# Kernel optimization log

Measured on AMD Instinct MI355X. Metric: run time of the kernel, lower is better.

## Reference

```python
import jax, jax.numpy as jnp
import numpy as np

B, T, ZS, ZT, H = 256, 256, 128, 64, 512
TAU = 1.0  # gumbel temperature


def setup_inputs() -> dict:
    key = jax.random.key(0)
    ks = iter(jax.random.split(key, 40))
    s = 0.05
    p = lambda shape: s * jax.random.normal(next(ks), shape, jnp.float32)
    return {
        'z_static': jax.random.normal(next(ks), (B, ZS), jnp.float32),
        'z_temporal': jax.random.normal(next(ks), (B, T, ZT), jnp.float32),
        'fc1_w': p((H, ZS)), 'fc1_b': p((H,)),
        'fc2_w': p((H, H)), 'fc2_b': p((H,)),
        'w_ih0': p((3 * H, ZT + H)), 'w_hh0': p((3 * H, H)), 'b_ih0': p((3 * H,)), 'b_hh0': p((3 * H,)),
        'w_ih1': p((3 * H, H)), 'w_hh1': p((3 * H, H)), 'b_ih1': p((3 * H,)), 'b_hh1': p((3 * H,)),
        'time_w': p((1, H)), 'time_b': p((1,)),
        'visit_w': p((1, H)), 'visit_b': p((1,)),
        'tcont_w': p((32, H)), 'tcont_b': p((32,)),
        'irr0_w': p((1, H)), 'irr0_b': p((1,)),
        'irr1_w': p((1, H)), 'irr1_b': p((1,)),
        'cat0_w': p((8, H)), 'cat0_b': p((8,)),
        'cat1_w': p((16, H)), 'cat1_b': p((16,)),
        'scont_w': p((16, H)), 'scont_b': p((16,)),
        'scat_w': p((10, H)), 'scat_b': p((10,)),
    }


def _gru_layer(x, w_ih, w_hh, b_ih, b_hh):
    # x: [B, T, in] -> [B, T, H]. PyTorch GRU gate order: r, z, n.
    xp = jnp.einsum('bti,gi->btg', x, w_ih) + b_ih  # [B,T,3H]
    h0 = jnp.zeros((x.shape[0], w_hh.shape[1]), x.dtype)

    def step(h, xpt):
        gh = h @ w_hh.T + b_hh
        ir, iz, inn = jnp.split(xpt, 3, axis=-1)
        hr, hz, hn = jnp.split(gh, 3, axis=-1)
        r = jax.nn.sigmoid(ir + hr)
        z = jax.nn.sigmoid(iz + hz)
        n = jnp.tanh(inn + r * hn)
        h = (1.0 - z) * n + z * h
        return h, h

    _, hs = jax.lax.scan(step, h0, xp.transpose(1, 0, 2))
    return hs.transpose(1, 0, 2)


def _gumbel_hard(k, logits, tau):
    u = jax.random.uniform(k, logits.shape, jnp.float32, 1e-9, 1.0)
    g = -jnp.log(-jnp.log(u))
    y = jax.nn.softmax((logits + g) / tau, axis=-1)
    hard = jax.nn.one_hot(jnp.argmax(y, axis=-1), logits.shape[-1], dtype=y.dtype)
    return hard + y - jax.lax.stop_gradient(y)  # straight-through


def _irr_scan(hazard, u):
    # hazard, u: [B, T] -> irreversible 0->1 states [B, T]
    def step(prev, hu):
        h, uu = hu
        flip = (uu < h * (1.0 - prev)).astype(h.dtype)
        prev = prev + flip
        return prev, prev

    _, st = jax.lax.scan(step, jnp.zeros(hazard.shape[0], hazard.dtype),
                         (hazard.T, u.T))
    return st.T


def reference(z_static, z_temporal, fc1_w, fc1_b, fc2_w, fc2_b,
              w_ih0, w_hh0, b_ih0, b_hh0, w_ih1, w_hh1, b_ih1, b_hh1,
              time_w, time_b, visit_w, visit_b, tcont_w, tcont_b,
              irr0_w, irr0_b, irr1_w, irr1_b, cat0_w, cat0_b, cat1_w, cat1_b,
              scont_w, scont_b, scat_w, scat_b):
    rk = jax.random.key(42)
    k_visit, k_i0, k_i1, k_c0, k_c1, k_sc = jax.random.split(rk, 6)

    static_h = jax.nn.relu(z_static @ fc1_w.T + fc1_b) @ fc2_w.T + fc2_b  # [B,H]
    gru_in = jnp.concatenate(
        [z_temporal, jnp.broadcast_to(static_h[:, None, :], (B, T, H))], axis=-1)
    h1 = _gru_layer(gru_in, w_ih0, w_hh0, b_ih0, b_hh0)
    h_seq = _gru_layer(h1, w_ih1, w_hh1, b_ih1, b_hh1)  # [B,T,H]

    static_cont = static_h @ scont_w.T + scont_b
    static_cat = _gumbel_hard(k_sc, static_h @ scat_w.T + scat_b, TAU)

    delta_t = jax.nn.softplus(jnp.squeeze(h_seq @ time_w.T + time_b, -1))  # [B,T]
    visit_times = jnp.cumsum(delta_t, axis=1)
    visit_times = visit_times / (jnp.max(visit_times, axis=1, keepdims=True) + 1e-8)

    visit_prob = jax.nn.sigmoid(jnp.squeeze(h_seq @ visit_w.T + visit_b, -1))
    u_visit = jax.random.uniform(k_visit, (B, T), jnp.float32)
    vm = (u_visit < visit_prob).astype(jnp.float32)
    vm = vm.at[:, 0].set(1.0)
    visit_mask = jnp.cumprod(vm, axis=1)[..., None]  # [B,T,1] monotone mask

    temporal_cont = (h_seq @ tcont_w.T + tcont_b) * visit_mask

    # irreversible categoricals via hazard recurrence
    def irr_out(w, b, k):
        hz = jax.nn.sigmoid(jnp.squeeze(h_seq @ w.T + b, -1))  # [B,T]
        st = _irr_scan(hz, jax.random.uniform(k, (B, T), jnp.float32))
        return jnp.stack([1.0 - st, st], axis=-1) * visit_mask  # [B,T,2]

    irr0 = irr_out(irr0_w, irr0_b, k_i0)
    irr1 = irr_out(irr1_w, irr1_b, k_i1)

    cat0 = _gumbel_hard(k_c0, h_seq @ cat0_w.T + cat0_b, TAU) * visit_mask
    cat1 = _gumbel_hard(k_c1, h_seq @ cat1_w.T + cat1_b, TAU) * visit_mask

    return (static_cont, static_cat, temporal_cont, irr0, irr1, cat0, cat1,
            visit_mask, visit_times)
```

## Files before the change

kernel.cpp:

```cpp
#include <hip/hip_runtime.h>
#include <hip/hip_bf16.h>
#include <cstdint>
#include <cstddef>

#define RNG_PART 1

typedef __bf16 bf16x8 __attribute__((ext_vector_type(8)));
typedef float f32x4 __attribute__((ext_vector_type(4)));
typedef unsigned short ushort_t;


static constexpr size_t ACC0 = 0;
static constexpr size_t SHH  = 393216;
static constexpr size_t HID  = 524288;
static constexpr size_t H0F  = 655360;
static constexpr size_t H1F  = 917504;
static constexpr size_t LOGB = 1179648;
static constexpr size_t WTH  = 5373952;
static constexpr size_t H0S  = 5406720;
static constexpr size_t H1S  = 5799936;
static constexpr size_t WB1  = 6193152;
static constexpr size_t WA0  = 8552448;
static constexpr size_t WH   = 9879552;
static constexpr size_t FC1T = LOGB;
static constexpr size_t FC2T = LOGB + 65536;
static constexpr size_t WIS  = FC2T + 262144;

static constexpr size_t O_SCONT = 0;
static constexpr size_t O_SCAT  = 4096;
static constexpr size_t O_TCONT = 6656;
static constexpr size_t O_IRR0  = 2103808;
static constexpr size_t O_IRR1  = 2234880;
static constexpr size_t O_CAT0  = 2365952;
static constexpr size_t O_CAT1  = 2890240;
static constexpr size_t O_VMASK = 3938816;
static constexpr size_t O_VTIME = 4004352;

__host__ __device__ inline void tf2x32(unsigned k0, unsigned k1, unsigned x0, unsigned x1,
                                       unsigned* o0, unsigned* o1) {
  unsigned ks2 = k0 ^ k1 ^ 0x1BD11BDAu;
#define TFR(r) { x0 += x1; x1 = (x1 << (r)) | (x1 >> (32 - (r))); x1 ^= x0; }
  x0 += k0; x1 += k1;
  TFR(13) TFR(15) TFR(26) TFR(6)
  x0 += k1; x1 += ks2 + 1u;
  TFR(17) TFR(29) TFR(16) TFR(24)
  x0 += ks2; x1 += k0 + 2u;
  TFR(13) TFR(15) TFR(26) TFR(6)
  x0 += k0; x1 += k1 + 3u;
  TFR(17) TFR(29) TFR(16) TFR(24)
  x0 += k1; x1 += ks2 + 4u;
  TFR(13) TFR(15) TFR(26) TFR(6)
  x0 += ks2; x1 += k0 + 5u;
#undef TFR
  *o0 = x0; *o1 = x1;
}

__device__ inline float rng_u01(unsigned k0, unsigned k1, unsigned idx) {
  unsigned o0, o1;
  tf2x32(k0, k1, 0u, idx, &o0, &o1);
  unsigned bits = o0 ^ o1;
  return __uint_as_float((bits >> 9) | 0x3f800000u) - 1.0f;
}

__device__ inline float sigmoidf_(float x) { return 1.0f / (1.0f + expf(-x)); }

__global__ __launch_bounds__(256) void transpose_k(const float* __restrict__ src, float* __restrict__ dst,
                                                   int J, int K, int srcStride, int dstStride) {
  __shared__ float tile[32][33];
  int kb = blockIdx.x * 32, jb = blockIdx.y * 32;
  int tx = threadIdx.x & 31, ty = threadIdx.x >> 5;
  #pragma unroll
  for (int r = 0; r < 4; ++r) {
    int j = jb + ty + r * 8, k = kb + tx;
    if (j < J && k < K) tile[ty + r * 8][tx] = src[(size_t)j * srcStride + k];
  }
  __syncthreads();
  #pragma unroll
  for (int r = 0; r < 4; ++r) {
    int k = kb + ty + r * 8, j = jb + tx;
    if (k < K && j < J) dst[(size_t)k * dstStride + j] = tile[tx][ty + r * 8];
  }
}

__global__ void hgather_k(const float* __restrict__ time_w, const float* __restrict__ visit_w,
                          const float* __restrict__ tcont_w, const float* __restrict__ irr0_w,
                          const float* __restrict__ irr1_w, const float* __restrict__ cat0_w,
                          const float* __restrict__ cat1_w, float* __restrict__ wtH) {
  int c = blockIdx.x;
  if (c >= 60) {
    for (int k = threadIdx.x; k < 512; k += blockDim.x) wtH[(size_t)k * 64 + c] = 0.0f;
    return;
  }
  const float* src;
  if (c == 0) src = time_w;
  else if (c == 1) src = visit_w;
  else if (c < 34) src = tcont_w + (size_t)(c - 2) * 512;
  else if (c == 34) src = irr0_w;
  else if (c == 35) src = irr1_w;
  else if (c < 44) src = cat0_w + (size_t)(c - 36) * 512;
  else src = cat1_w + (size_t)(c - 44) * 512;
  for (int k = threadIdx.x; k < 512; k += blockDim.x) wtH[(size_t)k * 64 + c] = src[k];
}

__global__ __launch_bounds__(128) void gemm_k(const float* __restrict__ in, const float* __restrict__ wT,
                                              const float* __restrict__ bias, float* __restrict__ out,
                                              int M, int K, int J, int relu) {
  __shared__ float ibuf[64][34];
  __shared__ float wbuf[64][36];
  int jt = blockIdx.x % (J >> 5), mt = blockIdx.x / (J >> 5);
  int m0 = mt * 32, j0 = jt * 32;
  int tid = threadIdx.x;
  int mq = tid & 15, jq = tid >> 4;
  float acc[2][4] = {{0.f, 0.f, 0.f, 0.f}, {0.f, 0.f, 0.f, 0.f}};
  for (int kc = 0; kc < K; kc += 64) {
    __syncthreads();
    #pragma unroll
    for (int i = 0; i < 16; ++i) {
      int lin = i * 128 + tid;
// ... 40 lines not shown
                                                   ushort_t* __restrict__ dst) {
  int id = blockIdx.x * 256 + threadIdx.x;
  if (id >= 32 * 32 * 3 * 64) return;
  int l = id & 63; int rest = id >> 6;
  int g = rest % 3; rest /= 3;
  int ht = rest & 31; int kc = rest >> 5;
  int n = g * 512 + ht * 16 + (l & 15);
  int kbase = kc * 32 + (l >> 4) * 8;
  size_t ob = (size_t)((kc * 32 + ht) * 3 + g) * 1536 + (size_t)l * 8;
  #pragma unroll
  for (int j = 0; j < 8; ++j) {
    int k = kbase + j;
    float v = (k < 512) ? w_ih1[(size_t)n * 512 + k] : w_hh1[(size_t)n * 512 + (k - 512)];
    split3_store(v, dst + ob + j, dst + ob + 512 + j, dst + ob + 1024 + j);
  }
}

__global__ __launch_bounds__(256) void arrangeA0_k(const float* __restrict__ w_hh0,
                                                   const float* __restrict__ w_ih0,
                                                   ushort_t* __restrict__ dst) {
  int id = blockIdx.x * 256 + threadIdx.x;
  if (id >= 18 * 32 * 3 * 64) return;
  int l = id & 63; int rest = id >> 6;
  int g = rest % 3; rest /= 3;
  int ht = rest & 31; int kc = rest >> 5;
  int n = g * 512 + ht * 16 + (l & 15);
  int kbase = kc * 32 + (l >> 4) * 8;
  size_t ob = (size_t)((kc * 32 + ht) * 3 + g) * 1536 + (size_t)l * 8;
  #pragma unroll
  for (int j = 0; j < 8; ++j) {
    int k = kbase + j;
    float v = (k < 512) ? w_hh0[(size_t)n * 512 + k] : w_ih0[(size_t)n * 576 + (k - 512)];
    split3_store(v, dst + ob + j, dst + ob + 512 + j, dst + ob + 1024 + j);
  }
}

__global__ __launch_bounds__(256) void arrangeH_k(const float* __restrict__ wtH,
                                                  ushort_t* __restrict__ dst) {
  int id = blockIdx.x * 256 + threadIdx.x;
  if (id >= 16 * 4 * 64) return;
  int l = id & 63; int rest = id >> 6;
  int ct = rest & 3; int kc = rest >> 2;
  int c = ct * 16 + (l & 15);
  int kbase = kc * 32 + (l >> 4) * 8;
  size_t ob = (size_t)(kc * 4 + ct) * 1536 + (size_t)l * 8;
  #pragma unroll
  for (int j = 0; j < 8; ++j) {
    float v = wtH[(size_t)(kbase + j) * 64 + c];
    split3_store(v, dst + ob + j, dst + ob + 512 + j, dst + ob + 1024 + j);
  }
}

__device__ inline bf16x8 ldb8(const ushort_t* p) { return *reinterpret_cast<const bf16x8*>(p); }

#define MFMA_(A, W, C) __builtin_amdgcn_mfma_f32_16x16x32_bf16((A), (W), (C), 0, 0, 0)

__device__ inline f32x4 mm6(f32x4 acc, bf16x8 a0, bf16x8 a1, bf16x8 a2, const ushort_t* wb) {
  bf16x8 w0 = ldb8(wb), w1 = ldb8(wb + 512), w2 = ldb8(wb + 1024);
  acc = MFMA_(a0, w0, acc); acc = MFMA_(a0, w1, acc); acc = MFMA_(a1, w0, acc);
  acc = MFMA_(a1, w1, acc); acc = MFMA_(a0, w2, acc); acc = MFMA_(a2, w0, acc);
  return acc;
}

struct HeadPtrs {
  const float *time_b, *visit_b, *tcont_b, *irr0_b, *irr1_b, *cat0_b, *cat1_b;
};

__device__ inline float head_bias(const HeadPtrs& hp, int c) {
  if (c == 0) return hp.time_b[0];
  if (c == 1) return hp.visit_b[0];
  if (c < 34) return hp.tcont_b[c - 2];
  if (c == 34) return hp.irr0_b[0];
  if (c == 35) return hp.irr1_b[0];
  if (c < 44) return hp.cat0_b[c - 36];
  return hp.cat1_b[c - 44];
}

__global__ __launch_bounds__(256, 2) void step_k(int s,
    const float* __restrict__ z_temporal,
    const float* __restrict__ b_hh0,
    const float* __restrict__ b_ih1, const float* __restrict__ b_hh1,
    float* __restrict__ ws, HeadPtrs hp)
{
  __shared__ f32x4 red[2][4][64];
  const int blk = blockIdx.x, tid = threadIdx.x;
  const int wv = tid >> 6, l = tid & 63, lm = l & 15, lq = l >> 4;
  const int mt = wv & 1, kh = wv >> 1;
  const ushort_t* h0sAll = (const ushort_t*)(ws + H0S);
  const ushort_t* h1sAll = (const ushort_t*)(ws + H1S);

  if (blk < 512) {
    const int job = blk & 1;
    const int idx = blk >> 1;
    const int ht = idx & 31, bt = idx >> 5;
    const int b0 = bt * 32 + mt * 16;
    const int hc = ht * 16;
    const size_t arow = (size_t)(b0 + lm) * 512 + (size_t)lq * 8;

    if (job == 0) {
      if (s < 1 || s > 256) return;
      const ushort_t* act = (kh == 0) ? (h0sAll + (size_t)((s - 1) & 1) * 393216)
                                      : (h1sAll + (size_t)(s & 1) * 393216);
      const ushort_t* wbB = (const ushort_t*)(ws + WB1) + (size_t)ht * 4608 + (size_t)l * 8
                            + (size_t)(kh * 16) * 147456;
      f32x4 vr = {}, vz = {}, vn = {};
      #pragma unroll 2
      for (int kcl = 0; kcl < 16; ++kcl) {
        const size_t ao = arow + (size_t)kcl * 32;
        bf16x8 a0 = ldb8(act + ao);
        bf16x8 a1 = ldb8(act + 131072 + ao);
        bf16x8 a2 = ldb8(act + 262144 + ao);
        const ushort_t* wb = wbB + (size_t)kcl * 147456;
        vr = mm6(vr, a0, a1, a2, wb);
        vz = mm6(vz, a0, a1, a2, wb + 1536);
        vn = mm6(vn, a0, a1, a2, wb + 3072);
      }
      if (kh == 1) { red[mt][0][l] = vr; red[mt][1][l] = vz; red[mt][2][l] = vn; }
      __syncthreads();
      if (kh == 0) {
        const f32x4 r4 = vr + red[mt][0][l];
        const f32x4 z4 = vz + red[mt][1][l];
        const f32x4 nh4 = red[mt][2][l];
        const float* h1f_old = ws + H1F + (size_t)(s & 1) * 131072;
        float* h1f_cur = ws + H1F + (size_t)((s - 1) & 1) * 131072;
        ushort_t* h1s_cur = (ushort_t*)(ws + H1S) + (size_t)((s - 1) & 1) * 393216;
        const int h = hc + lm;
        #pragma unroll
        for (int r = 0; r < 4; ++r) {
          const int b = b0 + lq * 4 + r;
          const float rr = r4[r] + b_ih1[h] + b_hh1[h];
          const float zz = z4[r] + b_ih1[512 + h] + b_hh1[512 + h];
          const float ni = vn[r] + b_ih1[1024 + h];
          const float nh = nh4[r] + b_hh1[1024 + h];
          const float rg = sigmoidf_(rr), zg = sigmoidf_(zz);
          const float n = tanhf(ni + rg * nh);
          const float hold = h1f_old[(size_t)b * 512 + h];
          const float hnew = (1.0f - zg) * n + zg * hold;
          h1f_cur[(size_t)b * 512 + h] = hnew;
          __bf16 t0 = (__bf16)hnew; float r1 = hnew - (float)t0;
          __bf16 t1 = (__bf16)r1;   float r2 = r1 - (float)t1;
          const size_t ho = (size_t)b * 512 + h;
          h1s_cur[ho]          = __builtin_bit_cast(ushort_t, t0);
          h1s_cur[131072 + ho] = __builtin_bit_cast(ushort_t, t1);
          h1s_cur[262144 + ho] = __builtin_bit_cast(ushort_t, (__bf16)r2);
        }
      }
    } else {
      if (s > 255) return;
      const ushort_t* act = h0sAll + (size_t)((s + 1) & 1) * 393216;
      const ushort_t* wbA = (const ushort_t*)(ws + WA0) + (size_t)ht * 4608 + (size_t)l * 8;
      f32x4 vr = {}, vz = {}, vn = {}, vni = {};
      const int nkc = kh ? 10 : 8;
      #pragma unroll 2
      for (int kcl = 0; kcl < nkc; ++kcl) {
        const int kcg = kh * 8 + kcl;
        bf16x8 a0, a1, a2;
        if (kcg < 16) {
          const size_t ao = arow + (size_t)kcg * 32;
          a0 = ldb8(act + ao);
          a1 = ldb8(act + 131072 + ao);
          a2 = ldb8(act + 262144 + ao);
        } else {
          const float* zp = z_temporal + ((size_t)(b0 + lm) * 256 + s) * 64 + (kcg - 16) * 32 + lq * 8;
          float4 q0 = *(const float4*)zp;
          float4 q1 = *(const float4*)(zp + 4);
          float vals[8] = {q0.x, q0.y, q0.z, q0.w, q1.x, q1.y, q1.z, q1.w};
          #pragma unroll
          for (int j = 0; j < 8; ++j) {
            float v = vals[j];
            __bf16 t0 = (__bf16)v; float r1 = v - (float)t0;
            __bf16 t1 = (__bf16)r1; float r2 = r1 - (float)t1;
            a0[j] = t0; a1[j] = t1; a2[j] = (__bf16)r2;
          }
        }
        const ushort_t* wb = wbA + (size_t)kcg * 147456;
        vr = mm6(vr, a0, a1, a2, wb);
        vz = mm6(vz, a0, a1, a2, wb + 1536);
        if (kcg < 16) vn  = mm6(vn,  a0, a1, a2, wb + 3072);
        else          vni = mm6(vni, a0, a1, a2, wb + 3072);
      }
      if (kh == 1) {
        red[mt][0][l] = vr; red[mt][1][l] = vz; red[mt][2][l] = vn; red[mt][3][l] = vni;
      }
      __syncthreads();
      if (kh == 0) {
        const f32x4 r4 = vr + red[mt][0][l];
        const f32x4 z4 = vz + red[mt][1][l];
        const f32x4 nh4 = vn + red[mt][2][l];
        const f32x4 ni4 = red[mt][3][l];
        const float* h0f_old = ws + H0F + (size_t)((s + 1) & 1) * 131072;
        float* h0f_cur = ws + H0F + (size_t)(s & 1) * 131072;
        ushort_t* h0s_cur = (ushort_t*)(ws + H0S) + (size_t)(s & 1) * 393216;
        const float* acc0 = ws + ACC0;
        const int h = hc + lm;
        #pragma unroll
        for (int r = 0; r < 4; ++r) {
          const int b = b0 + lq * 4 + r;
          const float* ac = acc0 + (size_t)b * 1536;
          const float rr = r4[r] + ac[h] + b_hh0[h];
          const float zz = z4[r] + ac[512 + h] + b_hh0[512 + h];
          const float ni = ni4[r] + ac[1024 + h];
          const float nh = nh4[r] + b_hh0[1024 + h];
          const float rg = sigmoidf_(rr), zg = sigmoidf_(zz);
          const float n = tanhf(ni + rg * nh);
          const float hold = h0f_old[(size_t)b * 512 + h];
          const float hnew = (1.0f - zg) * n + zg * hold;
          h0f_cur[(size_t)b * 512 + h] = hnew;
          __bf16 t0 = (__bf16)hnew; float r1 = hnew - (float)t0;
          __bf16 t1 = (__bf16)r1;   float r2 = r1 - (float)t1;
          const size_t ho = (size_t)b * 512 + h;
          h0s_cur[ho]          = __builtin_bit_cast(ushort_t, t0);
          h0s_cur[131072 + ho] = __builtin_bit_cast(ushort_t, t1);
          h0s_cur[262144 + ho] = __builtin_bit_cast(ushort_t, (__bf16)r2);
        }
      }
    }
  } else {
    if (s < 2) return;
    const int bt = blk - 512;
    const int b0 = bt * 32 + mt * 16;
    const int t = s - 2;
    const ushort_t* act = h1sAll + (size_t)(s & 1) * 393216;
    const ushort_t* wH = (const ushort_t*)(ws + WH) + (size_t)l * 8;
    const size_t arow = (size_t)(b0 + lm) * 512 + (size_t)lq * 8;
    f32x4 va[4] = {};
    #pragma unroll 2
    for (int kcl = 0; kcl < 8; ++kcl) {
      const int kc = kh * 8 + kcl;
      const size_t ao = arow + (size_t)kc * 32;
      bf16x8 a0 = ldb8(act + ao);
      bf16x8 a1 = ldb8(act + 131072 + ao);
      bf16x8 a2 = ldb8(act + 262144 + ao);
      #pragma unroll
      for (int ct = 0; ct < 4; ++ct)
        va[ct] = mm6(va[ct], a0, a1, a2, wH + (size_t)(kc * 4 + ct) * 1536);
    }
    if (kh == 1) {
      #pragma unroll
      for (int ct = 0; ct < 4; ++ct) red[mt][ct][l] = va[ct];
    }
    __syncthreads();
    if (kh == 0) {
      float* lg = ws + LOGB;
      #pragma unroll
      for (int ct = 0; ct < 4; ++ct) {
        const f32x4 v4 = va[ct] + red[mt][ct][l];
        const int c = ct * 16 + lm;
        if (c < 60) {
          const float bias = head_bias(hp, c);
          #pragma unroll
          for (int r = 0; r < 4; ++r) {
            const int b = b0 + lq * 4 + r;
            lg[((size_t)b * 256 + t) * 64 + c] = v4[r] + bias;
          }
        }
      }
    }
  }
}

__global__ __launch_bounds__(64) void static_heads_k(const float* __restrict__ sh_buf,
    const float* __restrict__ scont_w, const float* __restrict__ scont_b,
    const float* __restrict__ scat_w, const float* __restrict__ scat_b,
    float* __restrict__ out, unsigned ks0, unsigned ks1)
{
  __shared__ float hrow[512];
  __shared__ float xl[10];
  __shared__ float yv[10];
  __shared__ int argsh;
  int b = blockIdx.x, tid = threadIdx.x;
  const float* hr = sh_buf + (size_t)b * 512;
  for (int i = tid; i < 512; i += 64) hrow[i] = hr[i];
  __syncthreads();
  if (tid < 16) {
    float a = 0.f;
    const float* w = scont_w + (size_t)tid * 512;
    for (int k = 0; k < 512; ++k) a += hrow[k] * w[k];
    out[O_SCONT + (size_t)b * 16 + tid] = a + scont_b[tid];
  }
  if (tid < 10) {
    float a = 0.f;
    const float* w = scat_w + (size_t)tid * 512;
    for (int k = 0; k < 512; ++k) a += hrow[k] * w[k];
    a += scat_b[tid];
    float u = rng_u01(ks0, ks1, (unsigned)(b * 10 + tid));
    u = fmaxf(1e-9f, u + 1e-9f);
    float g = -logf(-logf(u));
    xl[tid] = a + g;
  }
  __syncthreads();
  if (tid == 0) {
    float m = xl[0];
    for (int c = 1; c < 10; ++c) m = fmaxf(m, xl[c]);
    float ssum = 0.f;
    for (int c = 0; c < 10; ++c) { yv[c] = expf(xl[c] - m); ssum += yv[c]; }
    int arg = 0; float best = -1.0f;
    for (int c = 0; c < 10; ++c) { yv[c] = yv[c] / ssum; if (yv[c] > best) { best = yv[c]; arg = c; } }
    argsh = arg;
  }
  __syncthreads();
  if (tid < 10) {
    float y = yv[tid];
    out[O_SCAT + (size_t)b * 10 + tid] = (tid == argsh) ? ((1.0f + y) - y) : 0.0f;
  }
}

struct Keys { unsigned kv0, kv1, ki00, ki01, ki10, ki11, kc00, kc01, kc10, kc11; };

__global__ __launch_bounds__(256) void final_k(const float* __restrict__ ws, float* __restrict__ out, Keys ky)
{
// ... 122 lines not shown
  const float* fc1_b = (const float*)d_in[3];
  const float* fc2_w = (const float*)d_in[4];
  const float* fc2_b = (const float*)d_in[5];
  const float* w_ih0 = (const float*)d_in[6];
  const float* w_hh0 = (const float*)d_in[7];
  const float* b_ih0 = (const float*)d_in[8];
  const float* b_hh0 = (const float*)d_in[9];
  const float* w_ih1 = (const float*)d_in[10];
  const float* w_hh1 = (const float*)d_in[11];
  const float* b_ih1 = (const float*)d_in[12];
  const float* b_hh1 = (const float*)d_in[13];
  const float* time_w = (const float*)d_in[14];
  const float* time_b = (const float*)d_in[15];
  const float* visit_w = (const float*)d_in[16];
  const float* visit_b = (const float*)d_in[17];
  const float* tcont_w = (const float*)d_in[18];
  const float* tcont_b = (const float*)d_in[19];
  const float* irr0_w = (const float*)d_in[20];
  const float* irr0_b = (const float*)d_in[21];
  const float* irr1_w = (const float*)d_in[22];
  const float* irr1_b = (const float*)d_in[23];
  const float* cat0_w = (const float*)d_in[24];
  const float* cat0_b = (const float*)d_in[25];
  const float* cat1_w = (const float*)d_in[26];
  const float* cat1_b = (const float*)d_in[27];
  const float* scont_w = (const float*)d_in[28];
  const float* scont_b = (const float*)d_in[29];
  const float* scat_w = (const float*)d_in[30];
  const float* scat_b = (const float*)d_in[31];
  float* ws = (float*)d_ws;
  float* out = (float*)d_out;

  transpose_k<<<dim3(4, 16), 256, 0, stream>>>(fc1_w, ws + FC1T, 512, 128, 128, 512);
  transpose_k<<<dim3(16, 16), 256, 0, stream>>>(fc2_w, ws + FC2T, 512, 512, 512, 512);
  transpose_k<<<dim3(16, 48), 256, 0, stream>>>(w_ih0 + 64, ws + WIS, 1536, 512, 576, 1536);
  hgather_k<<<64, 128, 0, stream>>>(time_w, visit_w, tcont_w, irr0_w, irr1_w, cat0_w, cat1_w, ws + WTH);

  gemm_k<<<8 * 16, 128, 0, stream>>>(z_static, ws + FC1T, fc1_b, ws + HID, 256, 128, 512, 1);
  gemm_k<<<8 * 16, 128, 0, stream>>>(ws + HID, ws + FC2T, fc2_b, ws + SHH, 256, 512, 512, 0);
  gemm_k<<<8 * 48, 128, 0, stream>>>(ws + SHH, ws + WIS, b_ih0, ws + ACC0, 256, 512, 1536, 0);

  arrangeB1_k<<<(32 * 32 * 3 * 64 + 255) / 256, 256, 0, stream>>>(w_ih1, w_hh1, (ushort_t*)(ws + WB1));
  arrangeA0_k<<<(18 * 32 * 3 * 64 + 255) / 256, 256, 0, stream>>>(w_hh0, w_ih0, (ushort_t*)(ws + WA0));
  arrangeH_k<<<(16 * 4 * 64 + 255) / 256, 256, 0, stream>>>(ws + WTH, (ushort_t*)(ws + WH));

  unsigned kk[6][2];
  for (int i = 0; i < 6; ++i) tf2x32(0u, 42u, 0u, (unsigned)i, &kk[i][0], &kk[i][1]);

  static_heads_k<<<256, 64, 0, stream>>>(ws + SHH, scont_w, scont_b, scat_w, scat_b, out,
                                         kk[5][0], kk[5][1]);

  hipMemsetAsync((void*)(ws + H0F + 131072), 0, 131072 * sizeof(float), stream);
  hipMemsetAsync((void*)(ws + H1F + 131072), 0, 131072 * sizeof(float), stream);
  hipMemsetAsync((void*)((ushort_t*)(ws + H0S) + 393216), 0, 393216 * sizeof(ushort_t), stream);
  hipMemsetAsync((void*)((ushort_t*)(ws + H1S) + 393216), 0, 393216 * sizeof(ushort_t), stream);

  HeadPtrs hp{time_b, visit_b, tcont_b, irr0_b, irr1_b, cat0_b, cat1_b};
  for (int s = 0; s <= 257; ++s)
    step_k<<<520, 256, 0, stream>>>(s, z_temporal, b_hh0, b_ih1, b_hh1, ws, hp);

  Keys ky{kk[0][0], kk[0][1], kk[1][0], kk[1][1], kk[2][0], kk[2][1],
          kk[3][0], kk[3][1], kk[4][0], kk[4][1]};
  final_k<<<256, 256, 0, stream>>>(ws, out, ky);
}
```

Before: 7.535 ms.

## Replace per-step kernel launches with a persistent kernel and a software grid barrier

The 258 per-timestep step_k launches become one persistent kernel of 256 blocks × 512 threads. Each block fuses the layer-1 job, the layer-0 job and a slice of the output-head GEMM, and blocks synchronise between steps with a hierarchical atomic grid barrier. This removes launch overhead and inter-kernel gaps on the serial recurrence. In exchange it depends on all 256 blocks being co-resident, and it spreads the head work across only 4 of the 32 ht tiles per batch tile, which adds imbalance.

```diff
diff --git a/kernel.cpp b/kernel.cpp
--- a/kernel.cpp
+++ b/kernel.cpp
@@ -2,8 +2,6 @@
 #include <hip/hip_bf16.h>
 #include <cstdint>
 #include <cstddef>
-
-#define RNG_PART 1
 
 typedef __bf16 bf16x8 __attribute__((ext_vector_type(8)));
 typedef float f32x4 __attribute__((ext_vector_type(4)));
@@ -22,6 +20,7 @@
 static constexpr size_t WB1  = 6193152;
 static constexpr size_t WA0  = 8552448;
 static constexpr size_t WH   = 9879552;
+static constexpr size_t BARO = 9928704;
 static constexpr size_t FC1T = LOGB;
 static constexpr size_t FC2T = LOGB + 65536;
 static constexpr size_t WIS  = FC2T + 262144;
@@ -210,7 +209,6 @@
 }
 
 __device__ inline bf16x8 ldb8(const ushort_t* p) { return *reinterpret_cast<const bf16x8*>(p); }
-
 #define MFMA_(A, W, C) __builtin_amdgcn_mfma_f32_16x16x32_bf16((A), (W), (C), 0, 0, 0)
 
 __device__ inline f32x4 mm6(f32x4 acc, bf16x8 a0, bf16x8 a1, bf16x8 a2, const ushort_t* wb) {
@@ -234,51 +232,141 @@
   return hp.cat1_b[c - 44];
 }
 
-__global__ __launch_bounds__(256, 2) void step_k(int s,
+__device__ inline void gridbar(unsigned* bar, unsigned* bgen) {
+  __syncthreads();
+  if (threadIdx.x == 0) {
+    __threadfence();
+    const unsigned g0 = *bgen;
+    const int cls = blockIdx.x & 7;
+    unsigned t = __hip_atomic_fetch_add(&bar[8 + cls], 1u, __ATOMIC_ACQ_REL, __HIP_MEMORY_SCOPE_AGENT);
+    bool done = false;
+    if (t == 31u) {
+      unsigned t2 = __hip_atomic_fetch_add(&bar[0], 1u, __ATOMIC_ACQ_REL, __HIP_MEMORY_SCOPE_AGENT);
+      if (t2 == 7u) {
+        #pragma unroll
+        for (int x = 0; x < 8; ++x)
+          __hip_atomic_store(&bar[8 + x], 0u, __ATOMIC_RELAXED, __HIP_MEMORY_SCOPE_AGENT);
+        __hip_atomic_store(&bar[0], 0u, __ATOMIC_RELAXED, __HIP_MEMORY_SCOPE_AGENT);
+        __threadfence();
+        __hip_atomic_fetch_add(&bar[1], 1u, __ATOMIC_ACQ_REL, __HIP_MEMORY_SCOPE_AGENT);
+        done = true;
+      }
+    }
+    if (!done) {
+      while (__hip_atomic_load(&bar[1], __ATOMIC_ACQUIRE, __HIP_MEMORY_SCOPE_AGENT) == g0)
+        __builtin_amdgcn_s_sleep(2);
+    }
+    __threadfence();
+    *bgen = g0 + 1u;
+  }
+  __syncthreads();
+}
+
+__global__ __launch_bounds__(512, 2) void persist_k(
     const float* __restrict__ z_temporal,
     const float* __restrict__ b_hh0,
     const float* __restrict__ b_ih1, const float* __restrict__ b_hh1,
     float* __restrict__ ws, HeadPtrs hp)
 {
-  __shared__ f32x4 red[2][4][64];
+  __shared__ f32x4 redB[2][3][64];
+  __shared__ f32x4 redA[2][4][64];
+  __shared__ f32x4 redC[2][64];
   const int blk = blockIdx.x, tid = threadIdx.x;
   const int wv = tid >> 6, l = tid & 63, lm = l & 15, lq = l >> 4;
-  const int mt = wv & 1, kh = wv >> 1;
+  const int bt = blk >> 5, ht = blk & 31;
+  const int roleA = (wv >= 4);
+  const int wq = wv & 3;
+  const int mt = wq & 1, kh = wq >> 1;
+  const int b0 = bt * 32 + mt * 16;
+  const int hc = ht * 16;
+  const size_t arow = (size_t)(b0 + lm) * 512 + (size_t)lq * 8;
+
   const ushort_t* h0sAll = (const ushort_t*)(ws + H0S);
   const ushort_t* h1sAll = (const ushort_t*)(ws + H1S);
-
-  if (blk < 512) {
-    const int job = blk & 1;
-    const int idx = blk >> 1;
-    const int ht = idx & 31, bt = idx >> 5;
-    const int b0 = bt * 32 + mt * 16;
-    const int hc = ht * 16;
-    const size_t arow = (size_t)(b0 + lm) * 512 + (size_t)lq * 8;
-
-    if (job == 0) {
-      if (s < 1 || s > 256) return;
-      const ushort_t* act = (kh == 0) ? (h0sAll + (size_t)((s - 1) & 1) * 393216)
-                                      : (h1sAll + (size_t)(s & 1) * 393216);
-      const ushort_t* wbB = (const ushort_t*)(ws + WB1) + (size_t)ht * 4608 + (size_t)l * 8
-                            + (size_t)(kh * 16) * 147456;
-      f32x4 vr = {}, vz = {}, vn = {};
-      #pragma unroll 2
-      for (int kcl = 0; kcl < 16; ++kcl) {
-        const size_t ao = arow + (size_t)kcl * 32;
-        bf16x8 a0 = ldb8(act + ao);
-        bf16x8 a1 = ldb8(act + 131072 + ao);
-        bf16x8 a2 = ldb8(act + 262144 + ao);
-        const ushort_t* wb = wbB + (size_t)kcl * 147456;
-        vr = mm6(vr, a0, a1, a2, wb);
-        vz = mm6(vz, a0, a1, a2, wb + 1536);
-        vn = mm6(vn, a0, a1, a2, wb + 3072);
+  unsigned* bar = (unsigned*)(ws + BARO);
+  unsigned bgen = 0;
+
+  for (int s = 0; s <= 257; ++s) {
+    f32x4 vr = {}, vz = {}, vn = {}, vni = {}, va = {};
+    if (!roleA) {
+      if (s >= 1 && s <= 256) {
+        const ushort_t* act = (kh == 0) ? (h0sAll + (size_t)((s - 1) & 1) * 393216)
+                                        : (h1sAll + (size_t)(s & 1) * 393216);
+        const ushort_t* wbB = (const ushort_t*)(ws + WB1) + (size_t)ht * 4608 + (size_t)l * 8
+                              + (size_t)(kh * 16) * 147456;
+        #pragma unroll 2
+        for (int kcl = 0; kcl < 16; ++kcl) {
+          const size_t ao = arow + (size_t)kcl * 32;
+          bf16x8 a0 = ldb8(act + ao);
+          bf16x8 a1 = ldb8(act + 131072 + ao);
+          bf16x8 a2 = ldb8(act + 262144 + ao);
+          const ushort_t* wb = wbB + (size_t)kcl * 147456;
+          vr = mm6(vr, a0, a1, a2, wb);
+          vz = mm6(vz, a0, a1, a2, wb + 1536);
+          vn = mm6(vn, a0, a1, a2, wb + 3072);
+        }
+        if (kh == 1) { redB[mt][0][l] = vr; redB[mt][1][l] = vz; redB[mt][2][l] = vn; }
       }
-      if (kh == 1) { red[mt][0][l] = vr; red[mt][1][l] = vz; red[mt][2][l] = vn; }
-      __syncthreads();
-      if (kh == 0) {
-        const f32x4 r4 = vr + red[mt][0][l];
-        const f32x4 z4 = vz + red[mt][1][l];
-        const f32x4 nh4 = red[mt][2][l];
+    } else {
+      if (s <= 255) {
+        const ushort_t* act = h0sAll + (size_t)((s + 1) & 1) * 393216;
+        const ushort_t* wbA = (const ushort_t*)(ws + WA0) + (size_t)ht * 4608 + (size_t)l * 8;
+        const int nkc = kh ? 10 : 8;
+        #pragma unroll 2
+        for (int kcl = 0; kcl < nkc; ++kcl) {
+          const int kcg = kh * 8 + kcl;
+          bf16x8 a0, a1, a2;
+          if (kcg < 16) {
+            const size_t ao = arow + (size_t)kcg * 32;
+            a0 = ldb8(act + ao);
+            a1 = ldb8(act + 131072 + ao);
+            a2 = ldb8(act + 262144 + ao);
+          } else {
+            const float* zp = z_temporal + ((size_t)(b0 + lm) * 256 + s) * 64 + (kcg - 16) * 32 + lq * 8;
+            float4 q0 = *(const float4*)zp;
+            float4 q1 = *(const float4*)(zp + 4);
+            float vals[8] = {q0.x, q0.y, q0.z, q0.w, q1.x, q1.y, q1.z, q1.w};
+            #pragma unroll
+            for (int j = 0; j < 8; ++j) {
+              float v = vals[j];
+              __bf16 t0 = (__bf16)v; float r1 = v - (float)t0;
+              __bf16 t1 = (__bf16)r1; float r2 = r1 - (float)t1;
+              a0[j] = t0; a1[j] = t1; a2[j] = (__bf16)r2;
+            }
+          }
+          const ushort_t* wb = wbA + (size_t)kcg * 147456;
+          vr = mm6(vr, a0, a1, a2, wb);
+          vz = mm6(vz, a0, a1, a2, wb + 1536);
+          if (kcg < 16) vn  = mm6(vn,  a0, a1, a2, wb + 3072);
+          else          vni = mm6(vni, a0, a1, a2, wb + 3072);
+        }
+        if (kh == 1) {
+          redA[mt][0][l] = vr; redA[mt][1][l] = vz; redA[mt][2][l] = vn; redA[mt][3][l] = vni;
+        }
+      }
+      if (ht < 4 && s >= 2) {
+        const ushort_t* actC = h1sAll + (size_t)(s & 1) * 393216;
+        const ushort_t* wH = (const ushort_t*)(ws + WH) + (size_t)l * 8;
+        #pragma unroll 2
+        for (int kcl = 0; kcl < 8; ++kcl) {
+          const int kc = kh * 8 + kcl;
+          const size_t ao = arow + (size_t)kc * 32;
+          bf16x8 a0 = ldb8(actC + ao);
+          bf16x8 a1 = ldb8(actC + 131072 + ao);
+          bf16x8 a2 = ldb8(actC + 262144 + ao);
+          va = mm6(va, a0, a1, a2, wH + (size_t)(kc * 4 + ht) * 1536);
+        }
+        if (kh == 1) redC[mt][l] = va;
+      }
+    }
+
+    __syncthreads();
+
+    if (!roleA) {
+      if (s >= 1 && s <= 256 && kh == 0) {
+        const f32x4 r4 = vr + redB[mt][0][l];
+        const f32x4 z4 = vz + redB[mt][1][l];
+        const f32x4 nh4 = redB[mt][2][l];
         const float* h1f_old = ws + H1F + (size_t)(s & 1) * 131072;
         float* h1f_cur = ws + H1F + (size_t)((s - 1) & 1) * 131072;
         ushort_t* h1s_cur = (ushort_t*)(ws + H1S) + (size_t)((s - 1) & 1) * 393216;
@@ -304,48 +392,11 @@
         }
       }
     } else {
-      if (s > 255) return;
-      const ushort_t* act = h0sAll + (size_t)((s + 1) & 1) * 393216;
-      const ushort_t* wbA = (const ushort_t*)(ws + WA0) + (size_t)ht * 4608 + (size_t)l * 8;
-      f32x4 vr = {}, vz = {}, vn = {}, vni = {};
-      const int nkc = kh ? 10 : 8;
-      #pragma unroll 2
-      for (int kcl = 0; kcl < nkc; ++kcl) {
-        const int kcg = kh * 8 + kcl;
-        bf16x8 a0, a1, a2;
-        if (kcg < 16) {
-          const size_t ao = arow + (size_t)kcg * 32;
-          a0 = ldb8(act + ao);
-          a1 = ldb8(act + 131072 + ao);
-          a2 = ldb8(act + 262144 + ao);
-        } else {
-          const float* zp = z_temporal + ((size_t)(b0 + lm) * 256 + s) * 64 + (kcg - 16) * 32 + lq * 8;
-          float4 q0 = *(const float4*)zp;
-          float4 q1 = *(const float4*)(zp + 4);
-          float vals[8] = {q0.x, q0.y, q0.z, q0.w, q1.x, q1.y, q1.z, q1.w};
-          #pragma unroll
-          for (int j = 0; j < 8; ++j) {
-            float v = vals[j];
-            __bf16 t0 = (__bf16)v; float r1 = v - (float)t0;
-            __bf16 t1 = (__bf16)r1; float r2 = r1 - (float)t1;
-            a0[j] = t0; a1[j] = t1; a2[j] = (__bf16)r2;
-          }
-        }
-        const ushort_t* wb = wbA + (size_t)kcg * 147456;
-        vr = mm6(vr, a0, a1, a2, wb);
-        vz = mm6(vz, a0, a1, a2, wb + 1536);
-        if (kcg < 16) vn  = mm6(vn,  a0, a1, a2, wb + 3072);
-        else          vni = mm6(vni, a0, a1, a2, wb + 3072);
-      }
-      if (kh == 1) {
-        red[mt][0][l] = vr; red[mt][1][l] = vz; red[mt][2][l] = vn; red[mt][3][l] = vni;
-      }
-      __syncthreads();
-      if (kh == 0) {
-        const f32x4 r4 = vr + red[mt][0][l];
-        const f32x4 z4 = vz + red[mt][1][l];
-        const f32x4 nh4 = vn + red[mt][2][l];
-        const f32x4 ni4 = red[mt][3][l];
+      if (s <= 255 && kh == 0) {
+        const f32x4 r4 = vr + redA[mt][0][l];
+        const f32x4 z4 = vz + redA[mt][1][l];
+        const f32x4 nh4 = vn + redA[mt][2][l];
+        const f32x4 ni4 = redA[mt][3][l];
         const float* h0f_old = ws + H0F + (size_t)((s + 1) & 1) * 131072;
         float* h0f_cur = ws + H0F + (size_t)(s & 1) * 131072;
         ushort_t* h0s_cur = (ushort_t*)(ws + H0S) + (size_t)(s & 1) * 393216;
@@ -372,40 +423,13 @@
           h0s_cur[262144 + ho] = __builtin_bit_cast(ushort_t, (__bf16)r2);
         }
       }
-    }
-  } else {
-    if (s < 2) return;
-    const int bt = blk - 512;
-    const int b0 = bt * 32 + mt * 16;
-    const int t = s - 2;
-    const ushort_t* act = h1sAll + (size_t)(s & 1) * 393216;
-    const ushort_t* wH = (const ushort_t*)(ws + WH) + (size_t)l * 8;
-    const size_t arow = (size_t)(b0 + lm) * 512 + (size_t)lq * 8;
-    f32x4 va[4] = {};
-    #pragma unroll 2
-    for (int kcl = 0; kcl < 8; ++kcl) {
-      const int kc = kh * 8 + kcl;
-      const size_t ao = arow + (size_t)kc * 32;
-      bf16x8 a0 = ldb8(act + ao);
-      bf16x8 a1 = ldb8(act + 131072 + ao);
-      bf16x8 a2 = ldb8(act + 262144 + ao);
-      #pragma unroll
-      for (int ct = 0; ct < 4; ++ct)
-        va[ct] = mm6(va[ct], a0, a1, a2, wH + (size_t)(kc * 4 + ct) * 1536);
-    }
-    if (kh == 1) {
-      #pragma unroll
-      for (int ct = 0; ct < 4; ++ct) red[mt][ct][l] = va[ct];
-    }
-    __syncthreads();
-    if (kh == 0) {
-      float* lg = ws + LOGB;
-      #pragma unroll
-      for (int ct = 0; ct < 4; ++ct) {
-        const f32x4 v4 = va[ct] + red[mt][ct][l];
-        const int c = ct * 16 + lm;
+      if (ht < 4 && s >= 2 && kh == 0) {
+        const f32x4 v4 = va + redC[mt][l];
+        const int t = s - 2;
+        const int c = ht * 16 + lm;
         if (c < 60) {
           const float bias = head_bias(hp, c);
+          float* lg = ws + LOGB;
           #pragma unroll
           for (int r = 0; r < 4; ++r) {
             const int b = b0 + lq * 4 + r;
@@ -414,6 +438,8 @@
         }
       }
     }
+
+    gridbar(bar, &bgen);
   }
 }
 
@@ -644,10 +670,10 @@
   hipMemsetAsync((void*)(ws + H1F + 131072), 0, 131072 * sizeof(float), stream);
   hipMemsetAsync((void*)((ushort_t*)(ws + H0S) + 393216), 0, 393216 * sizeof(ushort_t), stream);
   hipMemsetAsync((void*)((ushort_t*)(ws + H1S) + 393216), 0, 393216 * sizeof(ushort_t), stream);
+  hipMemsetAsync((void*)(ws + BARO), 0, 64, stream);
 
   HeadPtrs hp{time_b, visit_b, tcont_b, irr0_b, irr1_b, cat0_b, cat1_b};
-  for (int s = 0; s <= 257; ++s)
-    step_k<<<520, 256, 0, stream>>>(s, z_temporal, b_hh0, b_ih1, b_hh1, ws, hp);
+  persist_k<<<256, 512, 0, stream>>>(z_temporal, b_hh0, b_ih1, b_hh1, ws, hp);
 
   Keys ky{kk[0][0], kk[0][1], kk[1][0], kk[1][1], kk[2][0], kk[2][1],
           kk[3][0], kk[3][1], kk[4][0], kk[4][1]};
```

After: 18.40 ms. +144.2%, slower.

## Replace per-step kernel launches with persistent kernel and flat grid barrier

Applied to the files above, without the earlier changes.

Turns the 258 step_k launches into one persistent kernel of 512 blocks that loops over timesteps and uses a hand-rolled global atomic barrier between steps. The output-head GEMM is folded into the first four layer-0 job blocks, removing the extra 8 blocks. Hidden states are now kept only in fp32 and split into bf16 triples on load, so the separate split buffers and their writes are gone. This removes launch overhead and the split-buffer traffic. In exchange it adds system-scope atomic loads and stores, a spin barrier, and requires all 512 blocks to be co-resident, otherwise it deadlocks until the guard expires.

```diff
diff --git a/kernel.cpp b/kernel.cpp
--- a/kernel.cpp
+++ b/kernel.cpp
@@ -2,8 +2,6 @@
 #include <hip/hip_bf16.h>
 #include <cstdint>
 #include <cstddef>
-
-#define RNG_PART 1
 
 typedef __bf16 bf16x8 __attribute__((ext_vector_type(8)));
 typedef float f32x4 __attribute__((ext_vector_type(4)));
@@ -22,6 +20,7 @@
 static constexpr size_t WB1  = 6193152;
 static constexpr size_t WA0  = 8552448;
 static constexpr size_t WH   = 9879552;
+static constexpr size_t BARO = 9928704;
 static constexpr size_t FC1T = LOGB;
 static constexpr size_t FC2T = LOGB + 65536;
 static constexpr size_t WIS  = FC2T + 262144;
@@ -64,6 +63,17 @@
 
 __device__ inline float sigmoidf_(float x) { return 1.0f / (1.0f + expf(-x)); }
 
+__device__ inline unsigned long long cld64(const float* p) {
+  return __hip_atomic_load((const unsigned long long*)p, __ATOMIC_RELAXED, __HIP_MEMORY_SCOPE_SYSTEM);
+}
+__device__ inline float cldf(const float* p) {
+  unsigned u = __hip_atomic_load((const unsigned*)p, __ATOMIC_RELAXED, __HIP_MEMORY_SCOPE_SYSTEM);
+  return __uint_as_float(u);
+}
+__device__ inline void cstf(float* p, float v) {
+  __hip_atomic_store((unsigned*)p, __float_as_uint(v), __ATOMIC_RELAXED, __HIP_MEMORY_SCOPE_SYSTEM);
+}
+
 __global__ __launch_bounds__(256) void transpose_k(const float* __restrict__ src, float* __restrict__ dst,
                                                    int J, int K, int srcStride, int dstStride) {
   __shared__ float tile[32][33];
@@ -220,6 +230,16 @@
   return acc;
 }
 
+__device__ inline void split3v(const float* v8, bf16x8& a0, bf16x8& a1, bf16x8& a2) {
+  #pragma unroll
+  for (int j = 0; j < 8; ++j) {
+    float v = v8[j];
+    __bf16 t0 = (__bf16)v; float r1 = v - (float)t0;
+    __bf16 t1 = (__bf16)r1; float r2 = r1 - (float)t1;
+    a0[j] = t0; a1[j] = t1; a2[j] = (__bf16)r2;
+  }
+}
+
 struct HeadPtrs {
   const float *time_b, *visit_b, *tcont_b, *irr0_b, *irr1_b, *cat0_b, *cat1_b;
 };
@@ -234,102 +254,100 @@
   return hp.cat1_b[c - 44];
 }
 
-__global__ __launch_bounds__(256, 2) void step_k(int s,
+__device__ inline void flatbar(unsigned* arr, unsigned* go, int s, int blk, int tid) {
+  const unsigned gen = (unsigned)(s + 1);
+  __syncthreads();
+  asm volatile("s_waitcnt vmcnt(0)" ::: "memory");
+  if (tid == 0)
+    __hip_atomic_store(&arr[blk * 32], gen, __ATOMIC_RELAXED, __HIP_MEMORY_SCOPE_SYSTEM);
+  if (blk == 0) {
+    for (int i = tid; i < 512; i += 256) {
+      int guard = 0;
+      while (__hip_atomic_load(&arr[i * 32], __ATOMIC_RELAXED, __HIP_MEMORY_SCOPE_SYSTEM) < gen) {
+        __builtin_amdgcn_s_sleep(4);
+        if (++guard > 40000000) break;
+      }
+    }
+    __syncthreads();
+    if (tid == 0)
+      __hip_atomic_store(go, gen, __ATOMIC_RELAXED, __HIP_MEMORY_SCOPE_SYSTEM);
+  }
+  if (tid == 0) {
+    int guard = 0;
+    while (__hip_atomic_load(go, __ATOMIC_RELAXED, __HIP_MEMORY_SCOPE_SYSTEM) < gen) {
+      __builtin_amdgcn_s_sleep(2);
+      if (++guard > 40000000) break;
+    }
+  }
+  asm volatile("" ::: "memory");
+  __syncthreads();
+}
+
+__global__ __launch_bounds__(256, 2) void persist_k(
     const float* __restrict__ z_temporal,
     const float* __restrict__ b_hh0,
     const float* __restrict__ b_ih1, const float* __restrict__ b_hh1,
     float* __restrict__ ws, HeadPtrs hp)
 {
-  __shared__ f32x4 red[2][4][64];
+  __shared__ f32x4 red[2][5][64];
   const int blk = blockIdx.x, tid = threadIdx.x;
   const int wv = tid >> 6, l = tid & 63, lm = l & 15, lq = l >> 4;
   const int mt = wv & 1, kh = wv >> 1;
-  const ushort_t* h0sAll = (const ushort_t*)(ws + H0S);
-  const ushort_t* h1sAll = (const ushort_t*)(ws + H1S);
-
-  if (blk < 512) {
-    const int job = blk & 1;
-    const int idx = blk >> 1;
-    const int ht = idx & 31, bt = idx >> 5;
-    const int b0 = bt * 32 + mt * 16;
-    const int hc = ht * 16;
-    const size_t arow = (size_t)(b0 + lm) * 512 + (size_t)lq * 8;
-
-    if (job == 0) {
-      if (s < 1 || s > 256) return;
-      const ushort_t* act = (kh == 0) ? (h0sAll + (size_t)((s - 1) & 1) * 393216)
-                                      : (h1sAll + (size_t)(s & 1) * 393216);
+  const int job = blk & 1;
+  const int idx = blk >> 1;
+  const int ht = idx & 31, bt = idx >> 5;
+  const int b0 = bt * 32 + mt * 16;
+  const int hc = ht * 16;
+  const size_t arow = (size_t)(b0 + lm) * 512 + (size_t)lq * 8;
+  const bool doC = (job == 1) && (ht < 4);
+
+  float* h0f = ws + H0F;
+  float* h1f = ws + H1F;
+  unsigned* arr = (unsigned*)(ws + BARO);
+  unsigned* go  = arr + 512 * 32;
+
+  for (int s = 0; s <= 257; ++s) {
+    f32x4 vr = {}, vz = {}, vn = {}, vni = {}, va = {};
+    const bool actB = (job == 0) && s >= 1 && s <= 256;
+    const bool actA = (job == 1) && s <= 255;
+    const bool actC = doC && s >= 2;
+
+    if (actB) {
+      const float* act = (kh == 0) ? (h0f + (size_t)((s - 1) & 1) * 131072)
+                                   : (h1f + (size_t)(s & 1) * 131072);
       const ushort_t* wbB = (const ushort_t*)(ws + WB1) + (size_t)ht * 4608 + (size_t)l * 8
                             + (size_t)(kh * 16) * 147456;
-      f32x4 vr = {}, vz = {}, vn = {};
       #pragma unroll 2
       for (int kcl = 0; kcl < 16; ++kcl) {
-        const size_t ao = arow + (size_t)kcl * 32;
-        bf16x8 a0 = ldb8(act + ao);
-        bf16x8 a1 = ldb8(act + 131072 + ao);
-        bf16x8 a2 = ldb8(act + 262144 + ao);
+        const float* p = act + arow + (size_t)kcl * 32;
+        union { unsigned long long u[4]; float f[8]; } vv;
+        vv.u[0] = cld64(p); vv.u[1] = cld64(p + 2); vv.u[2] = cld64(p + 4); vv.u[3] = cld64(p + 6);
+        bf16x8 a0, a1, a2; split3v(vv.f, a0, a1, a2);
         const ushort_t* wb = wbB + (size_t)kcl * 147456;
         vr = mm6(vr, a0, a1, a2, wb);
         vz = mm6(vz, a0, a1, a2, wb + 1536);
         vn = mm6(vn, a0, a1, a2, wb + 3072);
       }
       if (kh == 1) { red[mt][0][l] = vr; red[mt][1][l] = vz; red[mt][2][l] = vn; }
-      __syncthreads();
-      if (kh == 0) {
-        const f32x4 r4 = vr + red[mt][0][l];
-        const f32x4 z4 = vz + red[mt][1][l];
-        const f32x4 nh4 = red[mt][2][l];
-        const float* h1f_old = ws + H1F + (size_t)(s & 1) * 131072;
-        float* h1f_cur = ws + H1F + (size_t)((s - 1) & 1) * 131072;
-        ushort_t* h1s_cur = (ushort_t*)(ws + H1S) + (size_t)((s - 1) & 1) * 393216;
-        const int h = hc + lm;
-        #pragma unroll
-        for (int r = 0; r < 4; ++r) {
-          const int b = b0 + lq * 4 + r;
-          const float rr = r4[r] + b_ih1[h] + b_hh1[h];
-          const float zz = z4[r] + b_ih1[512 + h] + b_hh1[512 + h];
-          const float ni = vn[r] + b_ih1[1024 + h];
-          const float nh = nh4[r] + b_hh1[1024 + h];
-          const float rg = sigmoidf_(rr), zg = sigmoidf_(zz);
-          const float n = tanhf(ni + rg * nh);
-          const float hold = h1f_old[(size_t)b * 512 + h];
-          const float hnew = (1.0f - zg) * n + zg * hold;
-          h1f_cur[(size_t)b * 512 + h] = hnew;
-          __bf16 t0 = (__bf16)hnew; float r1 = hnew - (float)t0;
-          __bf16 t1 = (__bf16)r1;   float r2 = r1 - (float)t1;
-          const size_t ho = (size_t)b * 512 + h;
-          h1s_cur[ho]          = __builtin_bit_cast(ushort_t, t0);
-          h1s_cur[131072 + ho] = __builtin_bit_cast(ushort_t, t1);
-          h1s_cur[262144 + ho] = __builtin_bit_cast(ushort_t, (__bf16)r2);
-        }
-      }
-    } else {
-      if (s > 255) return;
-      const ushort_t* act = h0sAll + (size_t)((s + 1) & 1) * 393216;
+    } else if (actA) {
+      const float* act = h0f + (size_t)((s + 1) & 1) * 131072;
       const ushort_t* wbA = (const ushort_t*)(ws + WA0) + (size_t)ht * 4608 + (size_t)l * 8;
-      f32x4 vr = {}, vz = {}, vn = {}, vni = {};
       const int nkc = kh ? 10 : 8;
       #pragma unroll 2
       for (int kcl = 0; kcl < nkc; ++kcl) {
         const int kcg = kh * 8 + kcl;
         bf16x8 a0, a1, a2;
         if (kcg < 16) {
-          const size_t ao = arow + (size_t)kcg * 32;
-          a0 = ldb8(act + ao);
-          a1 = ldb8(act + 131072 + ao);
-          a2 = ldb8(act + 262144 + ao);
+          const float* p = act + arow + (size_t)kcg * 32;
+          union { unsigned long long u[4]; float f[8]; } vv;
+          vv.u[0] = cld64(p); vv.u[1] = cld64(p + 2); vv.u[2] = cld64(p + 4); vv.u[3] = cld64(p + 6);
+          split3v(vv.f, a0, a1, a2);
         } else {
           const float* zp = z_temporal + ((size_t)(b0 + lm) * 256 + s) * 64 + (kcg - 16) * 32 + lq * 8;
           float4 q0 = *(const float4*)zp;
           float4 q1 = *(const float4*)(zp + 4);
           float vals[8] = {q0.x, q0.y, q0.z, q0.w, q1.x, q1.y, q1.z, q1.w};
-          #pragma unroll
-          for (int j = 0; j < 8; ++j) {
-            float v = vals[j];
-            __bf16 t0 = (__bf16)v; float r1 = v - (float)t0;
-            __bf16 t1 = (__bf16)r1; float r2 = r1 - (float)t1;
-            a0[j] = t0; a1[j] = t1; a2[j] = (__bf16)r2;
-          }
+          split3v(vals, a0, a1, a2);
         }
         const ushort_t* wb = wbA + (size_t)kcg * 147456;
         vr = mm6(vr, a0, a1, a2, wb);
@@ -340,80 +358,84 @@
       if (kh == 1) {
         red[mt][0][l] = vr; red[mt][1][l] = vz; red[mt][2][l] = vn; red[mt][3][l] = vni;
       }
-      __syncthreads();
-      if (kh == 0) {
-        const f32x4 r4 = vr + red[mt][0][l];
-        const f32x4 z4 = vz + red[mt][1][l];
-        const f32x4 nh4 = vn + red[mt][2][l];
-        const f32x4 ni4 = red[mt][3][l];
-        const float* h0f_old = ws + H0F + (size_t)((s + 1) & 1) * 131072;
-        float* h0f_cur = ws + H0F + (size_t)(s & 1) * 131072;
-        ushort_t* h0s_cur = (ushort_t*)(ws + H0S) + (size_t)(s & 1) * 393216;
-        const float* acc0 = ws + ACC0;
-        const int h = hc + lm;
+    }
+
+    if (actC) {
+      const float* actH = h1f + (size_t)(s & 1) * 131072;
+      const ushort_t* wH = (const ushort_t*)(ws + WH) + (size_t)l * 8;
+      #pragma unroll 2
+      for (int kcl = 0; kcl < 8; ++kcl) {
+        const int kc = kh * 8 + kcl;
+        const float* p = actH + arow + (size_t)kc * 32;
+        union { unsigned long long u[4]; float f[8]; } vv;
+        vv.u[0] = cld64(p); vv.u[1] = cld64(p + 2); vv.u[2] = cld64(p + 4); vv.u[3] = cld64(p + 6);
+        bf16x8 a0, a1, a2; split3v(vv.f, a0, a1, a2);
+        va = mm6(va, a0, a1, a2, wH + (size_t)(kc * 4 + ht) * 1536);
+      }
+      if (kh == 1) red[mt][4][l] = va;
+    }
+
+    __syncthreads();
+
+    if (actB && kh == 0) {
+      const f32x4 r4 = vr + red[mt][0][l];
+      const f32x4 z4 = vz + red[mt][1][l];
+      const f32x4 nh4 = red[mt][2][l];
+      const float* h1f_old = h1f + (size_t)(s & 1) * 131072;
+      float* h1f_cur = h1f + (size_t)((s - 1) & 1) * 131072;
+      const int h = hc + lm;
+      #pragma unroll
+      for (int r = 0; r < 4; ++r) {
+        const int b = b0 + lq * 4 + r;
+        const float rr = r4[r] + b_ih1[h] + b_hh1[h];
+        const float zz = z4[r] + b_ih1[512 + h] + b_hh1[512 + h];
+        const float ni = vn[r] + b_ih1[1024 + h];
+        const float nh = nh4[r] + b_hh1[1024 + h];
+        const float rg = sigmoidf_(rr), zg = sigmoidf_(zz);
+        const float n = tanhf(ni + rg * nh);
+        const float hold = cldf(&h1f_old[(size_t)b * 512 + h]);
+        cstf(&h1f_cur[(size_t)b * 512 + h], (1.0f - zg) * n + zg * hold);
+      }
+    } else if (actA && kh == 0) {
+      const f32x4 r4 = vr + red[mt][0][l];
+      const f32x4 z4 = vz + red[mt][1][l];
+      const f32x4 nh4 = vn + red[mt][2][l];
+      const f32x4 ni4 = red[mt][3][l];
+      const float* h0f_old = h0f + (size_t)((s + 1) & 1) * 131072;
+      float* h0f_cur = h0f + (size_t)(s & 1) * 131072;
+      const float* acc0 = ws + ACC0;
+      const int h = hc + lm;
+      #pragma unroll
+      for (int r = 0; r < 4; ++r) {
+        const int b = b0 + lq * 4 + r;
+        const float* ac = acc0 + (size_t)b * 1536;
+        const float rr = r4[r] + ac[h] + b_hh0[h];
+        const float zz = z4[r] + ac[512 + h] + b_hh0[512 + h];
+        const float ni = ni4[r] + ac[1024 + h];
+        const float nh = nh4[r] + b_hh0[1024 + h];
+        const float rg = sigmoidf_(rr), zg = sigmoidf_(zz);
+        const float n = tanhf(ni + rg * nh);
+        const float hold = cldf(&h0f_old[(size_t)b * 512 + h]);
+        cstf(&h0f_cur[(size_t)b * 512 + h], (1.0f - zg) * n + zg * hold);
+      }
+    }
+
+    if (actC && kh == 0) {
+      const f32x4 v4 = va + red[mt][4][l];
+      const int t = s - 2;
+      const int c = ht * 16 + lm;
+      if (c < 60) {
+        const float bias = head_bias(hp, c);
+        float* lg = ws + LOGB;
         #pragma unroll
         for (int r = 0; r < 4; ++r) {
           const int b = b0 + lq * 4 + r;
-          const float* ac = acc0 + (size_t)b * 1536;
-          const float rr = r4[r] + ac[h] + b_hh0[h];
-          const float zz = z4[r] + ac[512 + h] + b_hh0[512 + h];
-          const float ni = ni4[r] + ac[1024 + h];
-          const float nh = nh4[r] + b_hh0[1024 + h];
-          const float rg = sigmoidf_(rr), zg = sigmoidf_(zz);
-          const float n = tanhf(ni + rg * nh);
-          const float hold = h0f_old[(size_t)b * 512 + h];
-          const float hnew = (1.0f - zg) * n + zg * hold;
-          h0f_cur[(size_t)b * 512 + h] = hnew;
-          __bf16 t0 = (__bf16)hnew; float r1 = hnew - (float)t0;
-          __bf16 t1 = (__bf16)r1;   float r2 = r1 - (float)t1;
-          const size_t ho = (size_t)b * 512 + h;
-          h0s_cur[ho]          = __builtin_bit_cast(ushort_t, t0);
-          h0s_cur[131072 + ho] = __builtin_bit_cast(ushort_t, t1);
-          h0s_cur[262144 + ho] = __builtin_bit_cast(ushort_t, (__bf16)r2);
+          lg[((size_t)b * 256 + t) * 64 + c] = v4[r] + bias;
         }
       }
     }
-  } else {
-    if (s < 2) return;
-    const int bt = blk - 512;
-    const int b0 = bt * 32 + mt * 16;
-    const int t = s - 2;
-    const ushort_t* act = h1sAll + (size_t)(s & 1) * 393216;
-    const ushort_t* wH = (const ushort_t*)(ws + WH) + (size_t)l * 8;
-    const size_t arow = (size_t)(b0 + lm) * 512 + (size_t)lq * 8;
-    f32x4 va[4] = {};
-    #pragma unroll 2
-    for (int kcl = 0; kcl < 8; ++kcl) {
-      const int kc = kh * 8 + kcl;
-      const size_t ao = arow + (size_t)kc * 32;
-      bf16x8 a0 = ldb8(act + ao);
-      bf16x8 a1 = ldb8(act + 131072 + ao);
-      bf16x8 a2 = ldb8(act + 262144 + ao);
-      #pragma unroll
-      for (int ct = 0; ct < 4; ++ct)
-        va[ct] = mm6(va[ct], a0, a1, a2, wH + (size_t)(kc * 4 + ct) * 1536);
-    }
-    if (kh == 1) {
-      #pragma unroll
-      for (int ct = 0; ct < 4; ++ct) red[mt][ct][l] = va[ct];
-    }
-    __syncthreads();
-    if (kh == 0) {
-      float* lg = ws + LOGB;
-      #pragma unroll
-      for (int ct = 0; ct < 4; ++ct) {
-        const f32x4 v4 = va[ct] + red[mt][ct][l];
-        const int c = ct * 16 + lm;
-        if (c < 60) {
-          const float bias = head_bias(hp, c);
-          #pragma unroll
-          for (int r = 0; r < 4; ++r) {
-            const int b = b0 + lq * 4 + r;
-            lg[((size_t)b * 256 + t) * 64 + c] = v4[r] + bias;
-          }
-        }
-      }
-    }
+
+    flatbar(arr, go, s, blk, tid);
   }
 }
 
@@ -642,12 +664,10 @@
 
   hipMemsetAsync((void*)(ws + H0F + 131072), 0, 131072 * sizeof(float), stream);
   hipMemsetAsync((void*)(ws + H1F + 131072), 0, 131072 * sizeof(float), stream);
-  hipMemsetAsync((void*)((ushort_t*)(ws + H0S) + 393216), 0, 393216 * sizeof(ushort_t), stream);
-  hipMemsetAsync((void*)((ushort_t*)(ws + H1S) + 393216), 0, 393216 * sizeof(ushort_t), stream);
+  hipMemsetAsync((void*)(ws + BARO), 0, (512 * 32 + 64) * sizeof(unsigned), stream);
 
   HeadPtrs hp{time_b, visit_b, tcont_b, irr0_b, irr1_b, cat0_b, cat1_b};
-  for (int s = 0; s <= 257; ++s)
-    step_k<<<520, 256, 0, stream>>>(s, z_temporal, b_hh0, b_ih1, b_hh1, ws, hp);
+  persist_k<<<512, 256, 0, stream>>>(z_temporal, b_hh0, b_ih1, b_hh1, ws, hp);
 
   Keys ky{kk[0][0], kk[0][1], kk[1][0], kk[1][1], kk[2][0], kk[2][1],
           kk[3][0], kk[3][1], kk[4][0], kk[4][1]};
```

Result: slower. 7.987 ms (+6.0%).
